# Kernel tuning notes

Hardware: AMD Instinct MI355X
Metric: run time of the kernel (lower is better)

Reference implementation:

```python
import jax, jax.numpy as jnp
import numpy as np

GROUP = 8
BETA = 1.0
LOGVAR_MIN, LOGVAR_MAX = -30.0, 20.0
LOG2PI = float(np.log(2.0 * np.pi))


def setup_inputs() -> dict:
    key = jax.random.key(0)
    k1, k2 = jax.random.split(key)
    # z: [b, c, h, w] with c = 2*latent_c (mu/logvar halves)
    z = jax.random.normal(k1, (4, 64, 64, 64), dtype=jnp.float32)
    # stand-in for the scrambled-Sobol N(0,1) quasi-random codebook [n_samples, group]
    prior_samples = jax.random.normal(k2, (2048, GROUP), dtype=jnp.float32)
    return {"z": z, "prior_samples": prior_samples}


def reference(z, prior_samples):
    z = z.astype(jnp.float32)
    b, c, h, w = z.shape
    l = h * w
    z = z.reshape(b, c, l).transpose(0, 2, 1)          # b (h w) c
    c2 = c // 2
    mu, logvar = z[..., :c2], z[..., c2:]
    logvar = jnp.clip(logvar, LOGVAR_MIN, LOGVAR_MAX)
    std = jnp.exp(0.5 * logvar)
    ng = c2 // GROUP
    # [b, l, group, ng] -> [b, l, ng, group] -> [R, group],  R = b*l*ng
    mu_r = mu.reshape(b, l, GROUP, ng).transpose(0, 1, 3, 2).reshape(-1, GROUP)
    std_r = std.reshape(b, l, GROUP, ng).transpose(0, 1, 3, 2).reshape(-1, GROUP)

    s = prior_samples                                   # [N, G]
    s2 = s * s
    inv_var = 1.0 / (std_r * std_r)                     # [R, G]

    # sum_g Normal(0,1).log_prob(s) per codeword  -> [N]
    nlp_sum = jnp.sum(-0.5 * s2 - 0.5 * LOG2PI, axis=1)

    # score[r,n] = sum_g Normal(mu_r, std_r).log_prob(s[n]) - beta * nlp_sum[n]
    # expanded so the broadcast [R, N, G] tensor is never materialized:
    score = jnp.einsum('rg,ng->rn', -0.5 * inv_var, s2) \
          + jnp.einsum('rg,ng->rn', mu_r * inv_var, s)
    rowconst = (-0.5 * jnp.sum(mu_r * mu_r * inv_var, axis=1)
                - jnp.sum(jnp.log(std_r), axis=1)
                - 0.5 * GROUP * LOG2PI)                 # [R]
    score = score + rowconst[:, None] - BETA * nlp_sum[None, :]

    indices = jnp.argmax(score, axis=1)                 # [R]
    zhat = prior_samples[indices]                       # [R, G]

    zhat = zhat.reshape(b, l, ng, GROUP).transpose(0, 1, 3, 2).reshape(b, l, c2)
    indices = indices.reshape(b, l, ng)
    # back to bchw
    zhat = zhat.transpose(0, 2, 1).reshape(b, c2, h, w)
    indices = indices.transpose(0, 2, 1).reshape(b, ng, h, w)
    return zhat, indices
```

## Files before the change

### kernel.cpp

```cpp
#include <hip/hip_runtime.h>
#include <math.h>

#define L 4096
#define C2 32
#define CTOT 64
#define BB 4
#define NG 4
#define NSAMP 2048
#define SETSZ 512
#define NSETS (NSAMP / SETSZ)
#define NTILE (SETSZ / 16)
#define TPB 512
#define ROWSPB 128

typedef _Float16 half8 __attribute__((ext_vector_type(8)));
typedef float f32x4 __attribute__((ext_vector_type(4)));

__device__ __forceinline__ void split3(float x, _Float16& h, _Float16& m, _Float16& l) {
    h = (_Float16)x;
    float r1 = x - (float)h;
    m = (_Float16)r1;
    float r2 = r1 - (float)m;
    l = (_Float16)r2;
}

__global__ __launch_bounds__(TPB) void gqreg_kernel(
    const float* __restrict__ z, const float* __restrict__ prior,
    float* __restrict__ out )
{
    __shared__ _Float16 smem[NTILE * 6 * 16 * 8];
    char* sbase = (char*)smem;

    const int tid = threadIdx.x;
    const int lane = tid & 63;
    const int w = tid >> 6;
    const int i = lane & 15;
    const int kb = lane >> 4;

    const int r0 = blockIdx.x * ROWSPB + w * 16 + i;
    const int b0 = r0 >> 14, pos0 = (r0 >> 2) & (L - 1), ns0 = r0 & 3;
    const float* zb = z + (size_t)b0 * CTOT * L + pos0;

    half8 a_hm, a_hl;
    #pragma unroll
    for (int g = 0; g < 8; ++g) {
        float lv = zb[(size_t)(C2 + g * NG + ns0) * L];
        lv = fminf(fmaxf(lv, -30.f), 20.f);
        float iv = expf(-lv);
        float x;
        if (kb & 1) {
            float mu = zb[(size_t)(g * NG + ns0) * L];
            x = mu * iv;
        } else {
            x = 0.5f - 0.5f * iv;
        }
        _Float16 xh, xm, xl;
        split3(x, xh, xm, xl);
        a_hm[g] = (kb < 2) ? xh : xm;
        a_hl[g] = (kb < 2) ? xh : xl;
    }

    const int nl16 = i * 16;
    const int off1 = kb * 256 + nl16;
    const int off2 = (kb ^ 2) * 256 + nl16;
    const int off3 = ((kb < 2) ? (kb + 4) : (kb - 2)) * 256 + nl16;

    float best[4] = {-INFINITY, -INFINITY, -INFINITY, -INFINITY};
    int bidx[4] = {0, 0, 0, 0};
    const f32x4 zero4 = {0.f, 0.f, 0.f, 0.f};

    for (int set = 0; set < NSETS; ++set) {
        if (set > 0) __syncthreads();

        {
            int st = tid >> 4, snl = tid & 15;
            const float4* ps = (const float4*)(prior + (size_t)(set * SETSZ + tid) * 8);
            float4 u = ps[0], v = ps[1];
            float s[8] = {u.x, u.y, u.z, u.w, v.x, v.y, v.z, v.w};
            half8 qh, qm, ql, vh, vm, vl;
            #pragma unroll
            for (int g = 0; g < 8; ++g) {
                _Float16 h, m, l;
                split3(s[g] * s[g], h, m, l);
                qh[g] = h; qm[g] = m; ql[g] = l;
                split3(s[g], h, m, l);
                vh[g] = h; vm[g] = m; vl[g] = l;
            }
            char* tb = sbase + st * 1536 + snl * 16;
            *(half8*)(tb + 0 * 256) = qh;
            *(half8*)(tb + 1 * 256) = vh;
            *(half8*)(tb + 2 * 256) = qm;
            *(half8*)(tb + 3 * 256) = vm;
            *(half8*)(tb + 4 * 256) = ql;
            *(half8*)(tb + 5 * 256) = vl;
        }
        __syncthreads();

        int ncand = set * SETSZ + i;
        #pragma unroll
        for (int t = 0; t < NTILE; ++t) {
            const int tb = t * 1536;
            half8 f1 = *(const half8*)(sbase + tb + off1);
            half8 f2 = *(const half8*)(sbase + tb + off2);
            half8 f3 = *(const half8*)(sbase + tb + off3);
            f32x4 acc = __builtin_amdgcn_mfma_f32_16x16x32_f16(a_hm, f1, zero4, 0, 0, 0);
            acc = __builtin_amdgcn_mfma_f32_16x16x32_f16(a_hm, f2, acc, 0, 0, 0);
            acc = __builtin_amdgcn_mfma_f32_16x16x32_f16(a_hl, f3, acc, 0, 0, 0);
            #pragma unroll
            for (int j = 0; j < 4; ++j) {
                if (acc[j] > best[j]) { best[j] = acc[j]; bidx[j] = ncand; }
            }
            ncand += 16;
        }
    }

    #pragma unroll
    for (int j = 0; j < 4; ++j) {
        #pragma unroll
        for (int m = 1; m < 16; m <<= 1) {
            float os = __shfl_xor(best[j], m, 64);
            int oi = __shfl_xor(bidx[j], m, 64);
            if (os > best[j] || (os == best[j] && oi < bidx[j])) {
                best[j] = os; bidx[j] = oi;
            }
        }
    }

    if (i == 0) {
        #pragma unroll
        for (int j = 0; j < 4; ++j) {
            int rr = blockIdx.x * ROWSPB + w * 16 + kb * 4 + j;
            int b2 = rr >> 14, pos2 = (rr >> 2) & (L - 1), ns2 = rr & 3;
            int n = bidx[j];
            out[(size_t)BB * C2 * L + ((size_t)b2 * NG + ns2) * L + pos2] = (float)n;
            const float4* pn = (const float4*)(prior + (size_t)n * 8);
            float4 uu = pn[0], vv = pn[1];
            float sv[8] = {uu.x, uu.y, uu.z, uu.w, vv.x, vv.y, vv.z, vv.w};
            #pragma unroll
            for (int g = 0; g < 8; ++g) {
                out[((size_t)b2 * C2 + g * NG + ns2) * L + pos2] = sv[g];
            }
        }
    }
}

extern "C" void kernel_launch(void* const* d_in, const int* in_sizes, int n_in,
                              void* d_out, int out_size, void* d_ws, size_t ws_size,
                              hipStream_t stream) {
    const float* z = (const float*)d_in[0];
    const float* prior = (const float*)d_in[1];
    float* out = (float*)d_out;
    dim3 grid((BB * L * NG) / ROWSPB);
    dim3 block(TPB);
    hipLaunchKernelGGL(gqreg_kernel, grid, block, 0, stream, z, prior, out);
}
```

Baseline: 37.19 us.

## Switch to 32x32x16 MFMA with two row blocks per wave and prefetched prior sets

Replaces the 16x16x32 MFMA scheme with 32x32x16 MFMAs. Each wave now handles two 32-row blocks that share the B fragments, and six MFMAs build a split-fp16 product per tile. The block shrinks to 128 threads, sets are 256 candidates, and the next set's prior values are prefetched into registers while the current set is processed. The argmax needs more shuffle steps and the winning indices are redistributed through a small LDS buffer before output, which adds register pressure and extra MFMA work per tile.

```diff
diff --git a/kernel.cpp b/kernel.cpp
--- a/kernel.cpp
+++ b/kernel.cpp
@@ -7,14 +7,15 @@
 #define BB 4
 #define NG 4
 #define NSAMP 2048
-#define SETSZ 512
+#define SETSZ 256
 #define NSETS (NSAMP / SETSZ)
-#define NTILE (SETSZ / 16)
-#define TPB 512
+#define TPS (SETSZ / 32)
+#define TPB 128
+#define RB 2
 #define ROWSPB 128
 
 typedef _Float16 half8 __attribute__((ext_vector_type(8)));
-typedef float f32x4 __attribute__((ext_vector_type(4)));
+typedef float f32x16 __attribute__((ext_vector_type(16)));
 
 __device__ __forceinline__ void split3(float x, _Float16& h, _Float16& m, _Float16& l) {
     h = (_Float16)x;
@@ -28,117 +29,144 @@
     const float* __restrict__ z, const float* __restrict__ prior,
     float* __restrict__ out )
 {
-    __shared__ _Float16 smem[NTILE * 6 * 16 * 8];
-    char* sbase = (char*)smem;
+    __shared__ _Float16 smem[TPS * 1536];
+    __shared__ int ebuf[TPB / 64][2][16];
 
     const int tid = threadIdx.x;
     const int lane = tid & 63;
     const int w = tid >> 6;
-    const int i = lane & 15;
-    const int kb = lane >> 4;
+    const int col = lane & 31;
+    const int kh = lane >> 5;
+    char* sb = (char*)smem;
+    const float4* p4 = (const float4*)prior;
 
-    const int r0 = blockIdx.x * ROWSPB + w * 16 + i;
-    const int b0 = r0 >> 14, pos0 = (r0 >> 2) & (L - 1), ns0 = r0 & 3;
-    const float* zb = z + (size_t)b0 * CTOT * L + pos0;
-
-    half8 a_hm, a_hl;
-    #pragma unroll
-    for (int g = 0; g < 8; ++g) {
-        float lv = zb[(size_t)(C2 + g * NG + ns0) * L];
-        lv = fminf(fmaxf(lv, -30.f), 20.f);
-        float iv = expf(-lv);
-        float x;
-        if (kb & 1) {
-            float mu = zb[(size_t)(g * NG + ns0) * L];
-            x = mu * iv;
-        } else {
-            x = 0.5f - 0.5f * iv;
-        }
-        _Float16 xh, xm, xl;
-        split3(x, xh, xm, xl);
-        a_hm[g] = (kb < 2) ? xh : xm;
-        a_hl[g] = (kb < 2) ? xh : xl;
+    float4 pf0, pf1, pf2, pf3;
+    {
+        int n0 = tid, n1 = tid + TPB;
+        pf0 = p4[2 * n0]; pf1 = p4[2 * n0 + 1];
+        pf2 = p4[2 * n1]; pf3 = p4[2 * n1 + 1];
     }
 
-    const int nl16 = i * 16;
-    const int off1 = kb * 256 + nl16;
-    const int off2 = (kb ^ 2) * 256 + nl16;
-    const int off3 = ((kb < 2) ? (kb + 4) : (kb - 2)) * 256 + nl16;
+    const int rowbase = blockIdx.x * ROWSPB + w * (RB * 32);
+    half8 ah[RB], am[RB], al[RB];
+    #pragma unroll
+    for (int rb = 0; rb < RB; ++rb) {
+        int r = rowbase + rb * 32 + col;
+        int b = r >> 14, pos = (r >> 2) & (L - 1), ns = r & 3;
+        const float* zb = z + (size_t)b * CTOT * L + pos;
+        #pragma unroll
+        for (int g = 0; g < 8; ++g) {
+            float mu = zb[(size_t)(g * NG + ns) * L];
+            float lv = zb[(size_t)(C2 + g * NG + ns) * L];
+            lv = fminf(fmaxf(lv, -30.f), 20.f);
+            float iv = expf(-lv);
+            float x = kh ? (mu * iv) : (0.5f - 0.5f * iv);
+            _Float16 xh, xm, xl;
+            split3(x, xh, xm, xl);
+            ah[rb][g] = xh; am[rb][g] = xm; al[rb][g] = xl;
+        }
+    }
 
-    float best[4] = {-INFINITY, -INFINITY, -INFINITY, -INFINITY};
-    int bidx[4] = {0, 0, 0, 0};
-    const f32x4 zero4 = {0.f, 0.f, 0.f, 0.f};
+    const int lofs = kh * 512 + col * 16;
+
+    float best[RB][16];
+    int bidx[RB][16];
+    #pragma unroll
+    for (int rb = 0; rb < RB; ++rb)
+        #pragma unroll
+        for (int j = 0; j < 16; ++j) { best[rb][j] = -INFINITY; bidx[rb][j] = 0; }
+
+    const f32x16 z16 = {};
 
     for (int set = 0; set < NSETS; ++set) {
-        if (set > 0) __syncthreads();
-
-        {
-            int st = tid >> 4, snl = tid & 15;
-            const float4* ps = (const float4*)(prior + (size_t)(set * SETSZ + tid) * 8);
-            float4 u = ps[0], v = ps[1];
+        #pragma unroll
+        for (int ss = 0; ss < 2; ++ss) {
+            int nl = tid + ss * TPB;
+            float4 u = ss ? pf2 : pf0;
+            float4 v = ss ? pf3 : pf1;
             float s[8] = {u.x, u.y, u.z, u.w, v.x, v.y, v.z, v.w};
             half8 qh, qm, ql, vh, vm, vl;
             #pragma unroll
             for (int g = 0; g < 8; ++g) {
-                _Float16 h, m, l;
-                split3(s[g] * s[g], h, m, l);
-                qh[g] = h; qm[g] = m; ql[g] = l;
-                split3(s[g], h, m, l);
-                vh[g] = h; vm[g] = m; vl[g] = l;
+                _Float16 hh, mm, ll;
+                split3(s[g] * s[g], hh, mm, ll);
+                qh[g] = hh; qm[g] = mm; ql[g] = ll;
+                split3(s[g], hh, mm, ll);
+                vh[g] = hh; vm[g] = mm; vl[g] = ll;
             }
-            char* tb = sbase + st * 1536 + snl * 16;
-            *(half8*)(tb + 0 * 256) = qh;
-            *(half8*)(tb + 1 * 256) = vh;
-            *(half8*)(tb + 2 * 256) = qm;
-            *(half8*)(tb + 3 * 256) = vm;
-            *(half8*)(tb + 4 * 256) = ql;
-            *(half8*)(tb + 5 * 256) = vl;
+            char* tb = sb + (nl >> 5) * 3072 + (nl & 31) * 16;
+            *(half8*)(tb + 0)    = qh;
+            *(half8*)(tb + 512)  = vh;
+            *(half8*)(tb + 1024) = qm;
+            *(half8*)(tb + 1536) = vm;
+            *(half8*)(tb + 2048) = ql;
+            *(half8*)(tb + 2560) = vl;
+        }
+        if (set + 1 < NSETS) {
+            int n0 = (set + 1) * SETSZ + tid, n1 = n0 + TPB;
+            pf0 = p4[2 * n0]; pf1 = p4[2 * n0 + 1];
+            pf2 = p4[2 * n1]; pf3 = p4[2 * n1 + 1];
         }
         __syncthreads();
 
-        int ncand = set * SETSZ + i;
         #pragma unroll
-        for (int t = 0; t < NTILE; ++t) {
-            const int tb = t * 1536;
-            half8 f1 = *(const half8*)(sbase + tb + off1);
-            half8 f2 = *(const half8*)(sbase + tb + off2);
-            half8 f3 = *(const half8*)(sbase + tb + off3);
-            f32x4 acc = __builtin_amdgcn_mfma_f32_16x16x32_f16(a_hm, f1, zero4, 0, 0, 0);
-            acc = __builtin_amdgcn_mfma_f32_16x16x32_f16(a_hm, f2, acc, 0, 0, 0);
-            acc = __builtin_amdgcn_mfma_f32_16x16x32_f16(a_hl, f3, acc, 0, 0, 0);
+        for (int t = 0; t < TPS; ++t) {
+            const int tb = t * 3072;
+            half8 Bh = *(const half8*)(sb + tb + lofs);
+            half8 Bm = *(const half8*)(sb + tb + 1024 + lofs);
+            half8 Bl = *(const half8*)(sb + tb + 2048 + lofs);
+            int n = set * SETSZ + t * 32 + col;
             #pragma unroll
-            for (int j = 0; j < 4; ++j) {
-                if (acc[j] > best[j]) { best[j] = acc[j]; bidx[j] = ncand; }
+            for (int rb = 0; rb < RB; ++rb) {
+                f32x16 acc;
+                acc = __builtin_amdgcn_mfma_f32_32x32x16_f16(ah[rb], Bh, z16, 0, 0, 0);
+                acc = __builtin_amdgcn_mfma_f32_32x32x16_f16(ah[rb], Bm, acc, 0, 0, 0);
+                acc = __builtin_amdgcn_mfma_f32_32x32x16_f16(am[rb], Bh, acc, 0, 0, 0);
+                acc = __builtin_amdgcn_mfma_f32_32x32x16_f16(am[rb], Bm, acc, 0, 0, 0);
+                acc = __builtin_amdgcn_mfma_f32_32x32x16_f16(ah[rb], Bl, acc, 0, 0, 0);
+                acc = __builtin_amdgcn_mfma_f32_32x32x16_f16(al[rb], Bh, acc, 0, 0, 0);
+                #pragma unroll
+                for (int j = 0; j < 16; ++j) {
+                    if (acc[j] > best[rb][j]) { best[rb][j] = acc[j]; bidx[rb][j] = n; }
+                }
             }
-            ncand += 16;
+        }
+        __syncthreads();
+    }
+
+    #pragma unroll
+    for (int rb = 0; rb < RB; ++rb) {
+        #pragma unroll
+        for (int j = 0; j < 16; ++j) {
+            #pragma unroll
+            for (int m = 1; m < 32; m <<= 1) {
+                float os = __shfl_xor(best[rb][j], m, 64);
+                int oi = __shfl_xor(bidx[rb][j], m, 64);
+                if (os > best[rb][j] || (os == best[rb][j] && oi < bidx[rb][j])) {
+                    best[rb][j] = os; bidx[rb][j] = oi;
+                }
+            }
         }
     }
 
     #pragma unroll
-    for (int j = 0; j < 4; ++j) {
-        #pragma unroll
-        for (int m = 1; m < 16; m <<= 1) {
-            float os = __shfl_xor(best[j], m, 64);
-            int oi = __shfl_xor(bidx[j], m, 64);
-            if (os > best[j] || (os == best[j] && oi < bidx[j])) {
-                best[j] = os; bidx[j] = oi;
-            }
+    for (int rb = 0; rb < RB; ++rb) {
+        if (col == 0) {
+            #pragma unroll
+            for (int j = 0; j < 16; ++j) ebuf[w][kh][j] = bidx[rb][j];
         }
-    }
-
-    if (i == 0) {
-        #pragma unroll
-        for (int j = 0; j < 4; ++j) {
-            int rr = blockIdx.x * ROWSPB + w * 16 + kb * 4 + j;
-            int b2 = rr >> 14, pos2 = (rr >> 2) & (L - 1), ns2 = rr & 3;
-            int n = bidx[j];
-            out[(size_t)BB * C2 * L + ((size_t)b2 * NG + ns2) * L + pos2] = (float)n;
-            const float4* pn = (const float4*)(prior + (size_t)n * 8);
-            float4 uu = pn[0], vv = pn[1];
+        if (lane < 32) {
+            int half_ = (lane >> 4) & 1, j = lane & 15;
+            int n = ebuf[w][half_][j];
+            int row = (j & 3) + 8 * (j >> 2) + 4 * half_;
+            int r = rowbase + rb * 32 + row;
+            int b = r >> 14, pos = (r >> 2) & (L - 1), ns = r & 3;
+            out[(size_t)BB * C2 * L + ((size_t)b * NG + ns) * L + pos] = (float)n;
+            float4 uu = p4[2 * n], vv = p4[2 * n + 1];
             float sv[8] = {uu.x, uu.y, uu.z, uu.w, vv.x, vv.y, vv.z, vv.w};
             #pragma unroll
             for (int g = 0; g < 8; ++g) {
-                out[((size_t)b2 * C2 + g * NG + ns2) * L + pos2] = sv[g];
+                out[((size_t)b * C2 + g * NG + ns) * L + pos] = sv[g];
             }
         }
     }
```

Measured after the change: 65.40 us. +75.9%, slower.
